# Performance work log

Measured on AMD Instinct MI355X. Metric: run time of the kernel, lower is better.

## Reference

```python
import jax, jax.numpy as jnp
import numpy as np

B, S, E, H = 2, 2048, 1024, 16
D = E // H  # head dim = 64

def setup_inputs() -> dict:
    key = jax.random.key(0)
    ks = jax.random.split(key, 7)
    mk = lambda k, shape, scale=1.0: (jax.random.normal(k, shape, dtype=jnp.float32) * scale)
    return {
        "query": mk(ks[0], (B, S, E)),
        "key": mk(ks[1], (B, S, E)),
        "value": mk(ks[2], (B, S, E)),
        "Wq": mk(ks[3], (E, E), 1.0 / np.sqrt(E)),
        "Wk": mk(ks[4], (E, E), 1.0 / np.sqrt(E)),
        "Wv": mk(ks[5], (E, E), 1.0 / np.sqrt(E)),
        "Wo": mk(ks[6], (E, E), 1.0 / np.sqrt(E)),
    }

def reference(query, key, value, Wq, Wk, Wv, Wo):
    # nn.Linear(bias=False): y = x @ W.T
    def split_heads(x):
        return x.reshape(B, -1, H, D).transpose(0, 2, 1, 3)  # [B,H,S,D]
    q = split_heads(query @ Wq.T)
    k = split_heads(key @ Wk.T)
    v = split_heads(value @ Wv.T)
    scores = jnp.einsum("bhqd,bhkd->bhqk", q, k) / jnp.sqrt(jnp.float32(D))
    attn = jax.nn.softmax(scores, axis=-1)  # dropout p=0 -> identity
    out = jnp.einsum("bhqk,bhkd->bhqd", attn, v)
    out = out.transpose(0, 2, 1, 3).reshape(B, -1, E)
    out = out @ Wo.T
    return out
```

## Files before the change

kernel.cpp:

```cpp
#include <hip/hip_runtime.h>
#include <stdint.h>

#define S_LEN 2048
#define HDIM  64
#define EMB   1024
#define NTOK  4096

typedef short bf16x8 __attribute__((ext_vector_type(8)));
typedef float f32x4  __attribute__((ext_vector_type(4)));
typedef uint32_t u32x4 __attribute__((ext_vector_type(4)));
typedef uint32_t u32x2 __attribute__((ext_vector_type(2)));

__device__ __forceinline__ unsigned short f32_bf16(float f) {
  union { float f; uint32_t u; } v; v.f = f;
  return (unsigned short)((v.u + 0x7fffu + ((v.u >> 16) & 1u)) >> 16);
}

__device__ __forceinline__ uint32_t fbits(float f) {
  union { float f; uint32_t u; } v; v.f = f; return v.u;
}

__device__ __forceinline__ uint32_t pack_bf16_trunc(float lo, float hi) {
  return __builtin_amdgcn_perm(fbits(hi), fbits(lo), 0x07060302u);
}

__device__ __forceinline__ uint32_t pack_bf16_rne(float lo, float hi) {
  return (uint32_t)f32_bf16(lo) | ((uint32_t)f32_bf16(hi) << 16);
}

__device__ __forceinline__ void async_ld16(const unsigned short* g, unsigned short* l) {
  __builtin_amdgcn_global_load_lds(
      (__attribute__((address_space(1))) unsigned int*)(uintptr_t)g,
      (__attribute__((address_space(3))) unsigned int*)l, 16, 0, 0);
}

__device__ __forceinline__ void p_swap(uint32_t& x, uint32_t& y) {
  u32x2 r1 = __builtin_amdgcn_permlane32_swap(x, y, false, false);
  uint32_t a = r1[0], b = r1[1];
#if __has_builtin(__builtin_amdgcn_permlane16_swap)
  u32x2 r2 = __builtin_amdgcn_permlane16_swap(a, b, false, false);
  x = r2[0]; y = r2[1];
#else
  asm volatile("v_permlane16_swap_b32 %0, %1" : "+v"(a), "+v"(b));
  x = a; y = b;
#endif
}

#define CL2 0.18033688f

__global__ void cast_all(const float* __restrict__ q, const float* __restrict__ k,
                         const float* __restrict__ v, const float* __restrict__ Wq,
                         const float* __restrict__ Wk, const float* __restrict__ Wv,
                         const float* __restrict__ Wo,
                         unsigned short* __restrict__ qb, unsigned short* __restrict__ kb,
                         unsigned short* __restrict__ vb, unsigned short* __restrict__ wqb,
                         unsigned short* __restrict__ wkb, unsigned short* __restrict__ wvb,
                         unsigned short* __restrict__ wob) {
  const int b = blockIdx.x;
  const float* src; unsigned short* dst; int base;
  float scl = 1.0f;
  if (b < 12288) {
    const int which = b >> 12; base = b & 4095;
    src = which == 0 ? q : which == 1 ? k : v;
    dst = which == 0 ? qb : which == 1 ? kb : vb;
  } else {
    const int bb = b - 12288, which = bb >> 10; base = bb & 1023;
    src = which == 0 ? Wq : which == 1 ? Wk : which == 2 ? Wv : Wo;
    dst = which == 0 ? wqb : which == 1 ? wkb : which == 2 ? wvb : wob;
    if (which == 0) scl = CL2;
  }
  const int i = base * 256 + threadIdx.x;
  float4 f = ((const float4*)src)[i];
  ushort4 o;
  o.x = f32_bf16(f.x * scl); o.y = f32_bf16(f.y * scl);
  o.z = f32_bf16(f.z * scl); o.w = f32_bf16(f.w * scl);
  ((ushort4*)dst)[i] = o;
}

__global__ __launch_bounds__(256)
void gemm_qkv(const unsigned short* __restrict__ qb, const unsigned short* __restrict__ kb,
              const unsigned short* __restrict__ vb, const unsigned short* __restrict__ wqb,
              const unsigned short* __restrict__ wkb, const unsigned short* __restrict__ wvb,
              unsigned short* __restrict__ Qh, unsigned short* __restrict__ Kh,
              unsigned short* __restrict__ Vt) {
  __shared__ __align__(16) unsigned short As[2 * 128 * 32];
  __shared__ __align__(16) unsigned short Bs[2 * 128 * 32];

  const int z  = blockIdx.z;
  const int bx = blockIdx.y;
  const int by = blockIdx.x;
  const unsigned short* Xp = z == 0 ? qb  : z == 1 ? kb  : vb;
  const unsigned short* Wp = z == 0 ? wqb : z == 1 ? wkb : wvb;

  const unsigned short *A, *B;
  int tileM, tileN;
  if (z < 2) { A = Wp; tileM = bx * 128; B = Xp; tileN = by * 128; }
  else       { A = Xp; tileM = by * 128; B = Wp; tileN = bx * 128; }

  const int tid  = threadIdx.x;
  const int lane = tid & 63;
  const int wave = tid >> 6;
  const int wm = (wave >> 1) * 64;
  const int wn = (wave & 1) * 64;
  const int ccol = lane & 15;
  const int cgrp = lane >> 4;
  const int rchunk = lane >> 2;
  const int coff   = (lane & 3) * 8;

  f32x4 acc[4][4];
#pragma unroll
  for (int i = 0; i < 4; ++i)
#pragma unroll
    for (int j = 0; j < 4; ++j) acc[i][j] = 0.f;

  for (int k0 = 0; k0 < EMB; k0 += 64) {
#pragma unroll
    for (int kk = 0; kk < 2; ++kk)
#pragma unroll
      for (int i = 0; i < 2; ++i) {
        const int c = wave * 2 + i;
        const int row = c * 16 + rchunk;
        async_ld16(A + (size_t)(tileM + row) * EMB + k0 + kk * 32 + coff,
                   As + kk * 4096 + c * 512);
        async_ld16(B + (size_t)(tileN + row) * EMB + k0 + kk * 32 + coff,
                   Bs + kk * 4096 + c * 512);
      }
    __syncthreads();
#pragma unroll
    for (int kk = 0; kk < 2; ++kk) {
      bf16x8 af[4], bfm[4];
#pragma unroll
      for (int i = 0; i < 4; ++i) {
        af[i]  = *(const bf16x8*)(As + kk * 4096 + (wm + i * 16 + ccol) * 32 + cgrp * 8);
        bfm[i] = *(const bf16x8*)(Bs + kk * 4096 + (wn + i * 16 + ccol) * 32 + cgrp * 8);
      }
#pragma unroll
      for (int i = 0; i < 4; ++i)
#pragma unroll
        for (int j = 0; j < 4; ++j)
          acc[i][j] = __builtin_amdgcn_mfma_f32_16x16x32_bf16(af[i], bfm[j], acc[i][j], 0, 0, 0);
    }
    __syncthreads();
  }

  if (z < 2) {
    unsigned short* Oh = (z == 0) ? Qh : Kh;
#pragma unroll
    for (int i = 0; i < 4; ++i) {
      const int gd = tileM + wm + i * 16 + cgrp * 4;
      const int h = gd >> 6, dd = gd & 63;
#pragma unroll
      for (int j = 0; j < 4; ++j) {
        const int gt = tileN + wn + j * 16 + ccol;
        const int b = gt >> 11, s = gt & 2047;
        const uint32_t u0 = pack_bf16_rne(acc[i][j][0], acc[i][j][1]);
        const uint32_t u1 = pack_bf16_rne(acc[i][j][2], acc[i][j][3]);
        *(int2*)&Oh[((size_t)((b * 16 + h) * 2048 + s)) * 64 + dd] =
            make_int2((int)u0, (int)u1);
      }
    }
  } else {
#pragma unroll
    for (int i = 0; i < 4; ++i) {
      const int gt = tileM + wm + i * 16 + cgrp * 4;
      const int b = gt >> 11, s = gt & 2047;
#pragma unroll
      for (int j = 0; j < 4; ++j) {
        const int gd = tileN + wn + j * 16 + ccol;
        const int h = gd >> 6, dd = gd & 63;
        const uint32_t u0 = pack_bf16_rne(acc[i][j][0], acc[i][j][1]);
        const uint32_t u1 = pack_bf16_rne(acc[i][j][2], acc[i][j][3]);
        *(int2*)&Vt[((size_t)((b * 16 + h) * 64 + dd)) * 2048 + s] =
            make_int2((int)u0, (int)u1);
      }
    }
  }
}

__global__ __launch_bounds__(256)
void gemm_out(const unsigned short* __restrict__ Ctx, const unsigned short* __restrict__ Wo,
              float* __restrict__ Out) {
  __shared__ __align__(16) unsigned short As[2 * 64 * 32];
  __shared__ __align__(16) unsigned short Bs[2 * 128 * 32];

  const int tid  = threadIdx.x;
  const int lane = tid & 63;
  const int wave = tid >> 6;
  const int wm = (wave >> 1) * 32;
  const int wn = (wave & 1) * 64;
  const int ccol = lane & 15;
  const int cgrp = lane >> 4;
  const int rchunk = lane >> 2;
  const int coff   = (lane & 3) * 8;
  const int tileM = blockIdx.y * 64;
  const int tileN = blockIdx.x * 128;

  f32x4 acc[2][4];
#pragma unroll
  for (int i = 0; i < 2; ++i)
#pragma unroll
    for (int j = 0; j < 4; ++j) acc[i][j] = 0.f;

  for (int k0 = 0; k0 < EMB; k0 += 64) {
#pragma unroll
    for (int kk = 0; kk < 2; ++kk) {
      {
        const int row = wave * 16 + rchunk;
        async_ld16(Wo + (size_t)(tileM + row) * EMB + k0 + kk * 32 + coff,
                   As + kk * 2048 + wave * 512);
      }
#pragma unroll
      for (int i = 0; i < 2; ++i) {
        const int c = wave * 2 + i;
        const int row = c * 16 + rchunk;
        async_ld16(Ctx + (size_t)(tileN + row) * EMB + k0 + kk * 32 + coff,
                   Bs + kk * 4096 + c * 512);
      }
    }
    __syncthreads();
#pragma unroll
    for (int kk = 0; kk < 2; ++kk) {
      bf16x8 af[2], bfm[4];
#pragma unroll
      for (int i = 0; i < 2; ++i)
        af[i] = *(const bf16x8*)(As + kk * 2048 + (wm + i * 16 + ccol) * 32 + cgrp * 8);
#pragma unroll
      for (int j = 0; j < 4; ++j)
        bfm[j] = *(const bf16x8*)(Bs + kk * 4096 + (wn + j * 16 + ccol) * 32 + cgrp * 8);
#pragma unroll
      for (int i = 0; i < 2; ++i)
#pragma unroll
        for (int j = 0; j < 4; ++j)
          acc[i][j] = __builtin_amdgcn_mfma_f32_16x16x32_bf16(af[i], bfm[j], acc[i][j], 0, 0, 0);
    }
    __syncthreads();
  }

#pragma unroll
  for (int i = 0; i < 2; ++i) {
    const int odim = tileM + wm + i * 16 + cgrp * 4;
#pragma unroll
    for (int j = 0; j < 4; ++j) {
      const int gt = tileN + wn + j * 16 + ccol;
      float4 o = make_float4(acc[i][j][0], acc[i][j][1], acc[i][j][2], acc[i][j][3]);
      *(float4*)&Out[(size_t)gt * 1024 + odim] = o;
    }
  }
}

__global__ __launch_bounds__(256, 2)
void attn_kernel(const unsigned short* __restrict__ Qh,
                 const unsigned short* __restrict__ Kh,
                 const unsigned short* __restrict__ Vt,
                 unsigned short* __restrict__ Ctx) {
  __shared__ __align__(16) unsigned short Ks[2 * 64 * 64];
  __shared__ __align__(16) unsigned short Vs[2 * 64 * 64];
  __shared__ __align__(16) unsigned short Ps[128 * 64];

  const int tid  = threadIdx.x;
  const int lane = tid & 63;
  const int wave = tid >> 6;
  const int bh = blockIdx.x;
  const int q0 = blockIdx.y * 128;
  const unsigned short* Qg = Qh + ((size_t)bh * S_LEN + q0) * HDIM;
  const unsigned short* Kg = Kh + (size_t)bh * S_LEN * HDIM;
  const unsigned short* Vg = Vt + (size_t)bh * HDIM * S_LEN;

  const int ccol = lane & 15;
  const int cgrp = lane >> 4;
  const int mrow = wave * 32;
  const int sw7  = ccol & 7;

#pragma unroll
  for (int i = 0; i < 4; ++i) {
    const int cid = i * 256 + tid;
    const int row = cid >> 3, j = cid & 7, g = j ^ (row & 7);
    *(int4*)&Ps[row * 64 + j * 8] = *(const int4*)&Qg[(size_t)row * 64 + g * 8];
  }
  __syncthreads();
  bf16x8 aq[2][2];
#pragma unroll
  for (int g = 0; g < 2; ++g)
#pragma unroll
    for (int kk = 0; kk < 2; ++kk) {
      const int pp = (kk * 4 + cgrp) ^ sw7;
      aq[g][kk] = *(const bf16x8*)&Ps[(mrow + g * 16 + ccol) * 64 + pp * 8];
    }

  const int r0 = tid >> 3, j0 = tid & 7;
  const int r1 = r0 + 32;
  const int sA = j0 ^ (r0 & 7);
  const int sB = j0 ^ (r1 & 7);

  int4 kr0 = *(const int4*)&Kg[(size_t)r0 * 64 + sA * 8];
  int4 kr1 = *(const int4*)&Kg[(size_t)r1 * 64 + sB * 8];
  int4 vr0 = *(const int4*)&Vg[(size_t)r0 * 2048 + sA * 8];
  int4 vr1 = *(const int4*)&Vg[(size_t)r1 * 2048 + sB * 8];

  f32x4 l4[2];
  l4[0] = 0.f; l4[1] = 0.f;
  f32x4 o_acc[4][2];
#pragma unroll
  for (int dt = 0; dt < 4; ++dt) { o_acc[dt][0] = 0.f; o_acc[dt][1] = 0.f; }

  for (int i = 0; i < 32; ++i) {
    unsigned short* Kb = Ks + (i & 1) * 4096;
    unsigned short* Vb = Vs + (i & 1) * 4096;
    *(int4*)&Kb[r0 * 64 + j0 * 8] = kr0;
    *(int4*)&Kb[r1 * 64 + j0 * 8] = kr1;
    *(int4*)&Vb[r0 * 64 + j0 * 8] = vr0;
    *(int4*)&Vb[r1 * 64 + j0 * 8] = vr1;
    __syncthreads();
    if (i < 31) {
      const int nb = (i + 1) * 64;
      kr0 = *(const int4*)&Kg[(size_t)(nb + r0) * 64 + sA * 8];
      kr1 = *(const int4*)&Kg[(size_t)(nb + r1) * 64 + sB * 8];
      vr0 = *(const int4*)&Vg[(size_t)r0 * 2048 + nb + sA * 8];
      vr1 = *(const int4*)&Vg[(size_t)r1 * 2048 + nb + sB * 8];
    }

    f32x4 sc[2][4];
    __builtin_amdgcn_s_setprio(1);
#pragma unroll
    for (int nt = 0; nt < 4; ++nt) {
      const int krow = nt * 16 + ccol;
      bf16x8 ak0 = *(const bf16x8*)&Kb[krow * 64 + ((cgrp) ^ sw7) * 8];
      bf16x8 ak1 = *(const bf16x8*)&Kb[krow * 64 + ((4 + cgrp) ^ sw7) * 8];
#pragma unroll
      for (int g = 0; g < 2; ++g) {
        f32x4 s = 0.f;
        s = __builtin_amdgcn_mfma_f32_16x16x32_bf16(ak0, aq[g][0], s, 0, 0, 0);
        s = __builtin_amdgcn_mfma_f32_16x16x32_bf16(ak1, aq[g][1], s, 0, 0, 0);
        sc[g][nt] = s;
      }
    }
    __builtin_amdgcn_s_setprio(0);

#pragma unroll
    for (int g = 0; g < 2; ++g)
#pragma unroll
      for (int nt = 0; nt < 4; ++nt) {
#pragma unroll
        for (int r = 0; r < 4; ++r)
          sc[g][nt][r] = __builtin_amdgcn_exp2f(sc[g][nt][r]);
        l4[g] += sc[g][nt];
      }

    bf16x8 ap[2][2];
#pragma unroll
    for (int g = 0; g < 2; ++g) {
      uint32_t u[4][2];
#pragma unroll
      for (int nt = 0; nt < 4; ++nt) {
        u[nt][0] = pack_bf16_trunc(sc[g][nt][0], sc[g][nt][1]);
        u[nt][1] = pack_bf16_trunc(sc[g][nt][2], sc[g][nt][3]);
      }
      uint32_t w[2][4];
#pragma unroll
      for (int kk = 0; kk < 2; ++kk)
#pragma unroll
        for (int h = 0; h < 2; ++h) {
          uint32_t x = u[2 * kk][h], y = u[2 * kk + 1][h];
          p_swap(x, y);
          w[kk][h] = x; w[kk][2 + h] = y;
        }
#pragma unroll
      for (int kk = 0; kk < 2; ++kk) {
        union { u32x4 u; bf16x8 b; } cv;
        cv.u[0] = w[kk][0]; cv.u[1] = w[kk][1];
        cv.u[2] = w[kk][2]; cv.u[3] = w[kk][3];
        ap[g][kk] = cv.b;
      }
    }

    __builtin_amdgcn_s_setprio(1);
#pragma unroll
    for (int dt = 0; dt < 4; ++dt) {
      const int vrow = dt * 16 + ccol;
      bf16x8 av0 = *(const bf16x8*)&Vb[vrow * 64 + ((cgrp) ^ sw7) * 8];
      bf16x8 av1 = *(const bf16x8*)&Vb[vrow * 64 + ((4 + cgrp) ^ sw7) * 8];
#pragma unroll
      for (int g = 0; g < 2; ++g) {
        f32x4 o = o_acc[dt][g];
        o = __builtin_amdgcn_mfma_f32_16x16x32_bf16(av0, ap[g][0], o, 0, 0, 0);
        o = __builtin_amdgcn_mfma_f32_16x16x32_bf16(av1, ap[g][1], o, 0, 0, 0);
        o_acc[dt][g] = o;
      }
    }
    __builtin_amdgcn_s_setprio(0);
  }

  const int b = bh >> 4, h = bh & 15;
#pragma unroll
  for (int g = 0; g < 2; ++g) {
    float l_i = l4[g][0] + l4[g][1] + l4[g][2] + l4[g][3];
    l_i += __shfl_xor(l_i, 16);
    l_i += __shfl_xor(l_i, 32);
    const float inv_l = __builtin_amdgcn_rcpf(l_i) * 1.00195f;
    const int srow = q0 + mrow + g * 16 + ccol;
#pragma unroll
    for (int dt = 0; dt < 4; ++dt) {
      float o0 = o_acc[dt][g][0] * inv_l, o1 = o_acc[dt][g][1] * inv_l;
      float o2 = o_acc[dt][g][2] * inv_l, o3 = o_acc[dt][g][3] * inv_l;
      uint32_t u0 = pack_bf16_rne(o0, o1);
      uint32_t u1 = pack_bf16_rne(o2, o3);
      const int col = h * 64 + dt * 16 + cgrp * 4;
      *(int2*)&Ctx[((size_t)(b * 2048 + srow)) * 1024 + col] = make_int2((int)u0, (int)u1);
    }
  }
}

extern "C" void kernel_launch(void* const* d_in, const int* in_sizes, int n_in,
                              void* d_out, int out_size, void* d_ws, size_t ws_size,
                              hipStream_t stream) {
  const float* q  = (const float*)d_in[0];
  const float* k  = (const float*)d_in[1];
  const float* v  = (const float*)d_in[2];
  const float* Wq = (const float*)d_in[3];
  const float* Wk = (const float*)d_in[4];
  const float* Wv = (const float*)d_in[5];
  const float* Wo = (const float*)d_in[6];

  const size_t tok = (size_t)NTOK * EMB;
  const size_t wsz = (size_t)EMB * EMB;
  unsigned short* p = (unsigned short*)d_ws;
  unsigned short* qb  = p; p += tok;
  unsigned short* kb  = p; p += tok;
  unsigned short* vb  = p; p += tok;
  unsigned short* wqb = p; p += wsz;
  unsigned short* wkb = p; p += wsz;
  unsigned short* wvb = p; p += wsz;
  unsigned short* wob = p; p += wsz;
  unsigned short* Qh  = p; p += tok;
  unsigned short* Kh  = p; p += tok;
  unsigned short* Vt  = p; p += tok;
  unsigned short* Ctx = p; p += tok;

  cast_all<<<dim3(16384), dim3(256), 0, stream>>>(q, k, v, Wq, Wk, Wv, Wo,
                                                  qb, kb, vb, wqb, wkb, wvb, wob);

  gemm_qkv<<<dim3(32, 8, 3), dim3(256), 0, stream>>>(qb, kb, vb, wqb, wkb, wvb,
                                                     Qh, Kh, Vt);

  attn_kernel<<<dim3(32, 16), dim3(256), 0, stream>>>(Qh, Kh, Vt, Ctx);

  gemm_out<<<dim3(32, 16), dim3(256), 0, stream>>>(Ctx, wob, (float*)d_out);
}
```

Before: 205.6 us.

## Use async global-to-LDS loads and smaller attention blocks

The attention kernel now loads K and V tiles (and the initial Q tile) directly from global memory into shared memory with async loads, replacing the register-staged copy and the separate Q staging buffer. Each block now covers 64 queries with 2 waves instead of 128 queries with 4 waves, which doubles the grid size. The aim is to cut register pressure and VGPR-to-LDS store instructions and to get more blocks in flight. In exchange, every query block re-reads the full K/V for its head, so twice as many blocks stream the same K/V data, and the loop now waits for all outstanding loads at the end of each iteration.

Result: slower. 225.5 us (+9.7%).

```diff
diff --git a/kernel.cpp b/kernel.cpp
--- a/kernel.cpp
+++ b/kernel.cpp
@@ -248,20 +248,19 @@
   }
 }
 
-__global__ __launch_bounds__(256, 2)
+__global__ __launch_bounds__(128, 2)
 void attn_kernel(const unsigned short* __restrict__ Qh,
                  const unsigned short* __restrict__ Kh,
                  const unsigned short* __restrict__ Vt,
                  unsigned short* __restrict__ Ctx) {
   __shared__ __align__(16) unsigned short Ks[2 * 64 * 64];
   __shared__ __align__(16) unsigned short Vs[2 * 64 * 64];
-  __shared__ __align__(16) unsigned short Ps[128 * 64];
 
   const int tid  = threadIdx.x;
   const int lane = tid & 63;
   const int wave = tid >> 6;
   const int bh = blockIdx.x;
-  const int q0 = blockIdx.y * 128;
+  const int q0 = blockIdx.y * 64;
   const unsigned short* Qg = Qh + ((size_t)bh * S_LEN + q0) * HDIM;
   const unsigned short* Kg = Kh + (size_t)bh * S_LEN * HDIM;
   const unsigned short* Vg = Vt + (size_t)bh * HDIM * S_LEN;
@@ -271,31 +270,41 @@
   const int mrow = wave * 32;
   const int sw7  = ccol & 7;
 
-#pragma unroll
-  for (int i = 0; i < 4; ++i) {
-    const int cid = i * 256 + tid;
-    const int row = cid >> 3, j = cid & 7, g = j ^ (row & 7);
-    *(int4*)&Ps[row * 64 + j * 8] = *(const int4*)&Qg[(size_t)row * 64 + g * 8];
-  }
-  __syncthreads();
+  const int jj = tid & 7;
+  const int rr = tid >> 3;
+  int rA[4], gA[4];
+#pragma unroll
+  for (int cc = 0; cc < 4; ++cc) {
+    rA[cc] = cc * 16 + rr;
+    gA[cc] = (jj ^ (rA[cc] & 7)) * 8;
+  }
+  unsigned short* const KsW = Ks + wave * 512;
+  unsigned short* const VsW = Vs + wave * 512;
+
+#pragma unroll
+  for (int cc = 0; cc < 4; ++cc)
+    async_ld16(Qg + (size_t)rA[cc] * 64 + gA[cc], KsW + cc * 1024);
+  asm volatile("s_waitcnt vmcnt(0)" ::: "memory");
+  __builtin_amdgcn_s_barrier();
+
   bf16x8 aq[2][2];
 #pragma unroll
   for (int g = 0; g < 2; ++g)
 #pragma unroll
     for (int kk = 0; kk < 2; ++kk) {
       const int pp = (kk * 4 + cgrp) ^ sw7;
-      aq[g][kk] = *(const bf16x8*)&Ps[(mrow + g * 16 + ccol) * 64 + pp * 8];
-    }
-
-  const int r0 = tid >> 3, j0 = tid & 7;
-  const int r1 = r0 + 32;
-  const int sA = j0 ^ (r0 & 7);
-  const int sB = j0 ^ (r1 & 7);
-
-  int4 kr0 = *(const int4*)&Kg[(size_t)r0 * 64 + sA * 8];
-  int4 kr1 = *(const int4*)&Kg[(size_t)r1 * 64 + sB * 8];
-  int4 vr0 = *(const int4*)&Vg[(size_t)r0 * 2048 + sA * 8];
-  int4 vr1 = *(const int4*)&Vg[(size_t)r1 * 2048 + sB * 8];
+      aq[g][kk] = *(const bf16x8*)&Ks[(mrow + g * 16 + ccol) * 64 + pp * 8];
+    }
+  asm volatile("s_waitcnt lgkmcnt(0)" ::: "memory");
+  __builtin_amdgcn_s_barrier();
+
+#pragma unroll
+  for (int cc = 0; cc < 4; ++cc) {
+    async_ld16(Kg + (size_t)rA[cc] * 64 + gA[cc], KsW + cc * 1024);
+    async_ld16(Vg + (size_t)rA[cc] * 2048 + gA[cc], VsW + cc * 1024);
+  }
+  asm volatile("s_waitcnt vmcnt(0)" ::: "memory");
+  __builtin_amdgcn_s_barrier();
 
   f32x4 l4[2];
   l4[0] = 0.f; l4[1] = 0.f;
@@ -306,17 +315,16 @@
   for (int i = 0; i < 32; ++i) {
     unsigned short* Kb = Ks + (i & 1) * 4096;
     unsigned short* Vb = Vs + (i & 1) * 4096;
-    *(int4*)&Kb[r0 * 64 + j0 * 8] = kr0;
-    *(int4*)&Kb[r1 * 64 + j0 * 8] = kr1;
-    *(int4*)&Vb[r0 * 64 + j0 * 8] = vr0;
-    *(int4*)&Vb[r1 * 64 + j0 * 8] = vr1;
-    __syncthreads();
+
     if (i < 31) {
       const int nb = (i + 1) * 64;
-      kr0 = *(const int4*)&Kg[(size_t)(nb + r0) * 64 + sA * 8];
-      kr1 = *(const int4*)&Kg[(size_t)(nb + r1) * 64 + sB * 8];
-      vr0 = *(const int4*)&Vg[(size_t)r0 * 2048 + nb + sA * 8];
-      vr1 = *(const int4*)&Vg[(size_t)r1 * 2048 + nb + sB * 8];
+      unsigned short* KnW = Ks + ((i + 1) & 1) * 4096 + wave * 512;
+      unsigned short* VnW = Vs + ((i + 1) & 1) * 4096 + wave * 512;
+#pragma unroll
+      for (int cc = 0; cc < 4; ++cc) {
+        async_ld16(Kg + (size_t)(nb + rA[cc]) * 64 + gA[cc], KnW + cc * 1024);
+        async_ld16(Vg + (size_t)rA[cc] * 2048 + nb + gA[cc], VnW + cc * 1024);
+      }
     }
 
     f32x4 sc[2][4];
@@ -388,6 +396,9 @@
       }
     }
     __builtin_amdgcn_s_setprio(0);
+
+    asm volatile("s_waitcnt vmcnt(0) lgkmcnt(0)" ::: "memory");
+    __builtin_amdgcn_s_barrier();
   }
 
   const int b = bh >> 4, h = bh & 15;
@@ -442,7 +453,7 @@
   gemm_qkv<<<dim3(32, 8, 3), dim3(256), 0, stream>>>(qb, kb, vb, wqb, wkb, wvb,
                                                      Qh, Kh, Vt);
 
-  attn_kernel<<<dim3(32, 16), dim3(256), 0, stream>>>(Qh, Kh, Vt, Ctx);
+  attn_kernel<<<dim3(32, 32), dim3(128), 0, stream>>>(Qh, Kh, Vt, Ctx);
 
   gemm_out<<<dim3(32, 16), dim3(256), 0, stream>>>(Ctx, wob, (float*)d_out);
 }
```
